# Kernel optimization log

Measured on AMD Instinct MI355X. Metric: run time of the kernel, lower is better.

The kernel has to match this reference:

```python
import jax, jax.numpy as jnp
import numpy as np
import math

D_MODEL = 1024
N_HEAD = 16
D_HEAD = D_MODEL // N_HEAD
SCALE = math.sqrt(D_HEAD)
B, S = 8, 512


def setup_inputs() -> dict:
    key = jax.random.key(0)
    ks = jax.random.split(key, 7)
    x = jax.random.normal(ks[0], (B, S, D_MODEL), dtype=jnp.float32)
    mask = jnp.ones((B, S), dtype=jnp.int32)
    qmask = jax.random.randint(ks[1], (B, S), 0, 2).astype(jnp.int32)
    # params
    Wqkv = jax.random.normal(ks[2], (4 * D_MODEL, D_MODEL), dtype=jnp.float32) / math.sqrt(D_MODEL)
    fc_w = jax.random.normal(ks[3], (D_MODEL, D_MODEL), dtype=jnp.float32) / math.sqrt(D_MODEL)
    fc_b = jnp.zeros((D_MODEL,), dtype=jnp.float32)
    shift = jnp.abs(jax.random.normal(ks[4], (1,), dtype=jnp.float32)) + 0.001
    bias = -jnp.abs(jax.random.normal(ks[5], (1,), dtype=jnp.float32))
    return {"x": x, "mask": mask, "qmask": qmask, "Wqkv": Wqkv,
            "fc_w": fc_w, "fc_b": fc_b, "shift": shift, "bias": bias}


def reference(x, mask, qmask, Wqkv, fc_w, fc_b, shift, bias):
    Bsz, L, D = x.shape
    qkv = x @ Wqkv.T  # [B,S,4D], no bias
    q, k1, k2, v = jnp.split(qkv, 4, axis=-1)

    def heads(t):  # [B,S,D] -> [B,H,S,dh]
        return t.reshape(Bsz, L, N_HEAD, D_HEAD).transpose(0, 2, 1, 3)

    q, k1, k2, v = heads(q), heads(k1), heads(k2), heads(v)

    attn_self = jnp.einsum('bhqd,bhkd->bhqk', q, k1)
    attn_others = jnp.einsum('bhqd,bhkd->bhqk', q, k2)
    same_spk = (qmask[:, :, None] == qmask[:, None, :])[:, None]  # [B,1,S,S]
    attn = jnp.where(same_spk, attn_self, attn_others) / SCALE

    # key padding mask
    attn = jnp.where((mask == 0)[:, None, None, :], -jnp.inf, attn)

    # Gaussian distance bias: -(shift*(i-j)^2 + bias)
    pos = jnp.arange(L, dtype=jnp.float32)
    sq_dist = (pos[:, None] - pos[None, :]) ** 2  # [S,S]
    attn = attn - (shift[0] * sq_dist + bias[0])

    p = jax.nn.softmax(attn, axis=-1)  # dropout=0 (eval)
    out = jnp.einsum('bhqk,bhkd->bhqd', p, v)
    out = out.transpose(0, 2, 1, 3).reshape(Bsz, L, D)
    return out @ fc_w.T + fc_b
```

## Files before the change

kernel.cpp:

```cpp
#include <hip/hip_runtime.h>

typedef unsigned short u16;
typedef __bf16 bf16_t;
typedef bf16_t bf16x8 __attribute__((ext_vector_type(8)));
typedef float f32x4 __attribute__((ext_vector_type(4)));
typedef u16 u16x8 __attribute__((ext_vector_type(8)));
typedef u16 u16x4 __attribute__((ext_vector_type(4)));

__device__ __forceinline__ u16 f2b(float f) {
    unsigned int u = __float_as_uint(f);
    u += 0x7fffu + ((u >> 16) & 1u);
    return (u16)(u >> 16);
}

__device__ __forceinline__ f32x4 mfma16(u16x8 a, u16x8 b, f32x4 c) {
    return __builtin_amdgcn_mfma_f32_16x16x32_bf16(
        __builtin_bit_cast(bf16x8, a), __builtin_bit_cast(bf16x8, b), c, 0, 0, 0);
}

#define GLDS16(gp, lp)                                                          \
    __builtin_amdgcn_global_load_lds(                                           \
        (const __attribute__((address_space(1))) void*)(gp),                    \
        (__attribute__((address_space(3))) void*)(lp), 16, 0, 0)

__global__ __launch_bounds__(256) void cvt3_kernel(const float* __restrict__ s0,
                                                   const float* __restrict__ s1,
                                                   const float* __restrict__ s2,
                                                   u16* __restrict__ d0,
                                                   u16* __restrict__ d1,
                                                   u16* __restrict__ d2) {
    int i = (blockIdx.x * 256 + threadIdx.x) * 4;
    const float* src; u16* dst;
    if (i < 4194304)       { src = s0;           dst = d0;           }
    else if (i < 8388608)  { src = s1 - 4194304; dst = d1 - 4194304; }
    else                   { src = s2 - 8388608; dst = d2 - 8388608; }
    float4 f = *(const float4*)(src + i);
    u16x4 o = { f2b(f.x), f2b(f.y), f2b(f.z), f2b(f.w) };
    *(u16x4*)(dst + i) = o;
}

template <int MT, int MODE>
__global__ __launch_bounds__(256) void gemm_bt(
    const u16* __restrict__ A, const u16* __restrict__ Bw,
    u16* __restrict__ Qf, u16* __restrict__ K1f,
    u16* __restrict__ K2f, u16* __restrict__ Vf,
    float* __restrict__ Cf, const float* __restrict__ biasp)
{
    constexpr int K = 1024;
    constexpr int MF = MT / 32;
    __shared__ u16 As[2][MT * 32];
    __shared__ u16 Bs[2][128 * 32];
    const int t = threadIdx.x;
    const int lane = t & 63;
    const int w = t >> 6;
    const int wm = w >> 1, wn = w & 1;
    const int lr = lane & 15, quad = lane >> 4;
    const int tileM = blockIdx.y * MT, tileN = blockIdx.x * 128;

    f32x4 acc[MF][4] = {};

    const u16* Ag = A + (size_t)(tileM + (t >> 2)) * K + (t & 3) * 8;
    const u16* Bg = Bw + (size_t)(tileN + (t >> 2)) * K + (t & 3) * 8;

#define STAGE(kk, bufi)                                                         \
    do {                                                                        \
        GLDS16(Ag + (kk), &As[bufi][t * 8]);                                    \
        if (MT == 128) GLDS16(Ag + (kk) + 64 * K, &As[bufi][t * 8 + 2048]);     \
        GLDS16(Bg + (kk), &Bs[bufi][t * 8]);                                    \
        GLDS16(Bg + (kk) + 64 * K, &Bs[bufi][t * 8 + 2048]);                    \
    } while (0)

    STAGE(0, 0);
    __syncthreads();

#pragma unroll 2
    for (int kk = 0; kk < K; kk += 32) {
        const int cur = (kk >> 5) & 1;
        if (kk + 32 < K) STAGE(kk + 32, cur ^ 1);

        u16x8 af[MF], bf[4];
#pragma unroll
        for (int i = 0; i < MF; ++i)
            af[i] = *(const u16x8*)(&As[cur][(wm * (MT / 2) + i * 16 + lr) * 32 + quad * 8]);
#pragma unroll
        for (int i = 0; i < 4; ++i)
            bf[i] = *(const u16x8*)(&Bs[cur][(wn * 64 + i * 16 + lr) * 32 + quad * 8]);
#pragma unroll
        for (int mi = 0; mi < MF; ++mi)
#pragma unroll
            for (int ni = 0; ni < 4; ++ni)
                acc[mi][ni] = mfma16(af[mi], bf[ni], acc[mi][ni]);

        __syncthreads();
    }
#undef STAGE

    if (MODE == 0) {
#pragma unroll
        for (int mi = 0; mi < MF; ++mi)
#pragma unroll
            for (int ni = 0; ni < 4; ++ni) {
                int n = tileN + wn * 64 + ni * 16 + lr;
                int kv = n >> 10;
                int h = (n >> 6) & 15, d = n & 63;
#pragma unroll
                for (int r = 0; r < 4; ++r) {
                    int m = tileM + wm * (MT / 2) + mi * 16 + quad * 4 + r;
                    int s = m & 511, bh = ((m >> 9) << 4) + h;
                    u16 v = f2b(acc[mi][ni][r]);
                    if (kv < 3) {
                        u16* base = (kv == 0) ? Qf : (kv == 1) ? K1f : K2f;
                        size_t idx = ((size_t)((bh * 32 + (s >> 4)) * 2 + (d >> 5))) * 512
                                   + (((d >> 3) & 3) * 16 + (s & 15)) * 8 + (d & 7);
                        base[idx] = v;
                    } else {
                        size_t idx = ((size_t)((bh * 4 + (d >> 4)) * 16 + (s >> 5))) * 512
                                   + (((s >> 3) & 3) * 16 + (d & 15)) * 8 + (s & 7);
                        Vf[idx] = v;
                    }
                }
            }
    } else {
#pragma unroll
        for (int mi = 0; mi < MF; ++mi)
#pragma unroll
            for (int ni = 0; ni < 4; ++ni) {
                int n = tileN + wn * 64 + ni * 16 + lr;
                float bv = biasp[n];
#pragma unroll
                for (int r = 0; r < 4; ++r) {
                    int m = tileM + wm * (MT / 2) + mi * 16 + quad * 4 + r;
                    Cf[(size_t)m * 1024 + n] = acc[mi][ni][r] + bv;
                }
            }
    }
}

__global__ __launch_bounds__(256) void attn_kernel(
    const u16* __restrict__ qfm, const u16* __restrict__ k1fm,
    const u16* __restrict__ k2fm, const u16* __restrict__ vfm,
    const int* __restrict__ maskp, const int* __restrict__ qmaskp,
    const float* __restrict__ shiftp, const float* __restrict__ biasp,
    u16* __restrict__ ao)
{
    __shared__ u16 Pw[4][2][512];

    const int bh = blockIdx.x & 127, qt = blockIdx.x >> 7;
    const int b = bh >> 4, h = bh & 15;
    const int t = threadIdx.x, lane = t & 63, w = t >> 6;
    const int lr = lane & 15, quad = lane >> 4;
    const float shiftv = shiftp[0], biasv = biasp[0];

    const int qbase = qt * 128 + w * 32;
    const int m16 = qbase >> 4;

    const u16* qb = qfm + ((size_t)(bh * 32 + m16) * 2) * 512 + lane * 8;
    u16x8 qa[2][2];
    qa[0][0] = *(const u16x8*)(qb);
    qa[0][1] = *(const u16x8*)(qb + 512);
    qa[1][0] = *(const u16x8*)(qb + 1024);
    qa[1][1] = *(const u16x8*)(qb + 1536);

    int qmr[2][4]; float rowf[2][4];
#pragma unroll
    for (int g = 0; g < 2; ++g)
#pragma unroll
        for (int r = 0; r < 4; ++r) {
            int m = qbase + g * 16 + quad * 4 + r;
            qmr[g][r] = qmaskp[b * 512 + m];
            rowf[g][r] = (float)m;
        }

    f32x4 o[2][4] = {};
    float lsum[2][4] = {};

    u16* pb[2] = { &Pw[w][0][0], &Pw[w][1][0] };
    const int wa0 = quad * 128 + (((lr >> 3) ^ quad) * 8) + (lr & 7);
    const int wa1 = quad * 128 + (((2 | (lr >> 3)) ^ quad) * 8) + (lr & 7);
    const int ra = lr * 32 + ((quad ^ (lr >> 2)) * 8);

    const u16* k1b = k1fm + (size_t)bh * 32768 + lane * 8;
    const u16* k2b = k2fm + (size_t)bh * 32768 + lane * 8;
    const u16* vb  = vfm  + (size_t)bh * 32768 + lane * 8;
    const int* qmb = qmaskp + b * 512;
    const int* kmb = maskp + b * 512;

#pragma unroll 2
    for (int cc = 0; cc < 16; ++cc) {
        const u16* kc1 = k1b + cc * 2048;
        const u16* kc2 = k2b + cc * 2048;
        u16x8 k1f_[2][2], k2f_[2][2];
        k1f_[0][0] = *(const u16x8*)(kc1);
        k1f_[0][1] = *(const u16x8*)(kc1 + 512);
        k1f_[1][0] = *(const u16x8*)(kc1 + 1024);
        k1f_[1][1] = *(const u16x8*)(kc1 + 1536);
        k2f_[0][0] = *(const u16x8*)(kc2);
        k2f_[0][1] = *(const u16x8*)(kc2 + 512);
        k2f_[1][0] = *(const u16x8*)(kc2 + 1024);
        k2f_[1][1] = *(const u16x8*)(kc2 + 1536);
        u16x8 vf_[4];
#pragma unroll
        for (int ot = 0; ot < 4; ++ot)
            vf_[ot] = *(const u16x8*)(vb + (size_t)(ot * 16 + cc) * 512);

        f32x4 z = {0.f, 0.f, 0.f, 0.f};
        f32x4 s1[2][2], s2[2][2];
#pragma unroll
        for (int g = 0; g < 2; ++g)
#pragma unroll
            for (int tg = 0; tg < 2; ++tg) {
                s1[g][tg] = mfma16(qa[g][1], k1f_[tg][1], mfma16(qa[g][0], k1f_[tg][0], z));
                s2[g][tg] = mfma16(qa[g][1], k2f_[tg][1], mfma16(qa[g][0], k2f_[tg][0], z));
            }

        const int col0 = cc * 32 + lr, col1 = col0 + 16;
        const int qmc0 = qmb[col0], qmc1 = qmb[col1];
        const float ka0 = (kmb[col0] ? 0.f : -1e30f) - 10.0f;
        const float ka1 = (kmb[col1] ? 0.f : -1e30f) - 10.0f;
        const float colf0 = (float)col0, colf1 = (float)col1;

#pragma unroll
        for (int g = 0; g < 2; ++g) {
#pragma unroll
            for (int r = 0; r < 4; ++r) {
                float d0 = rowf[g][r] - colf0;
                float d1 = rowf[g][r] - colf1;
                float sel0 = (qmr[g][r] == qmc0) ? s1[g][0][r] : s2[g][0][r];
                float sel1 = (qmr[g][r] == qmc1) ? s1[g][1][r] : s2[g][1][r];
                float v0 = fmaf(sel0, 0.125f, -fmaf(shiftv * d0, d0, biasv)) + ka0;
                float v1 = fmaf(sel1, 0.125f, -fmaf(shiftv * d1, d1, biasv)) + ka1;
                float p0 = __expf(v0);
                float p1 = __expf(v1);
                lsum[g][r] += p0 + p1;
                pb[g][wa0 + r * 32] = f2b(p0);
                pb[g][wa1 + r * 32] = f2b(p1);
            }
        }
#pragma unroll
        for (int g = 0; g < 2; ++g) {
            u16x8 af = *(const u16x8*)(pb[g] + ra);
#pragma unroll
            for (int ot = 0; ot < 4; ++ot)
                o[g][ot] = mfma16(af, vf_[ot], o[g][ot]);
        }
    }

#pragma unroll
    for (int g = 0; g < 2; ++g)
#pragma unroll
        for (int r = 0; r < 4; ++r) {
            float s = lsum[g][r];
#pragma unroll
            for (int m = 1; m < 16; m <<= 1) s += __shfl_xor(s, m);
            float inv = 1.0f / s;
            int grow = b * 512 + qbase + g * 16 + quad * 4 + r;
            u16* orow = ao + (size_t)grow * 1024 + h * 64 + lr;
            orow[0]  = f2b(o[g][0][r] * inv);
            orow[16] = f2b(o[g][1][r] * inv);
            orow[32] = f2b(o[g][2][r] * inv);
            orow[48] = f2b(o[g][3][r] * inv);
        }
}

extern "C" void kernel_launch(void* const* d_in, const int* in_sizes, int n_in,
                              void* d_out, int out_size, void* d_ws, size_t ws_size,
                              hipStream_t stream) {
    (void)in_sizes; (void)n_in; (void)out_size; (void)ws_size;
    const float* x      = (const float*)d_in[0];
    const int*   maskp  = (const int*)d_in[1];
    const int*   qmaskp = (const int*)d_in[2];
    const float* Wqkv   = (const float*)d_in[3];
    const float* fc_w   = (const float*)d_in[4];
    const float* fc_b   = (const float*)d_in[5];
    const float* shiftp = (const float*)d_in[6];
    const float* biasp  = (const float*)d_in[7];
    float* out = (float*)d_out;

    char* ws = (char*)d_ws;
    u16* xb   = (u16*)(ws);
    u16* wb   = (u16*)(ws + (8u << 20));
    u16* fwb  = (u16*)(ws + (16u << 20));
    u16* qfm  = (u16*)(ws + (18u << 20));
    u16* k1fm = (u16*)(ws + (26u << 20));
    u16* k2fm = (u16*)(ws + (34u << 20));
    u16* vfm  = (u16*)(ws + (42u << 20));
    u16* aob  = (u16*)(ws + (50u << 20));

    cvt3_kernel<<<9216, 256, 0, stream>>>(x, Wqkv, fc_w, xb, wb, fwb);
    gemm_bt<128, 0><<<dim3(32, 32), 256, 0, stream>>>(xb, wb, qfm, k1fm, k2fm, vfm,
                                                      nullptr, nullptr);
    attn_kernel<<<512, 256, 0, stream>>>(qfm, k1fm, k2fm, vfm, maskp, qmaskp,
                                         shiftp, biasp, aob);
    gemm_bt<64, 1><<<dim3(8, 64), 256, 0, stream>>>(aob, fwb, nullptr, nullptr,
                                                    nullptr, nullptr, out, fc_b);
}
```

Measured before the change: 205.0 us.

## Swap GEMM operand roles for QKV tiles to write packed bf16 fragments

In the QKV projection GEMM, blocks producing Q/K1/K2 swap which shared-memory tile feeds the A and B MFMA operands, so each lane's accumulator holds consecutive head-dim elements. Lanes can then pack four bf16 values into one 8-byte store instead of scattered 2-byte stores. The V blocks likewise use vectorized packed stores, and the attention kernel's fragment-layout addressing changes to match the new intermediate layout. This targets the costly scattered epilogue writes in the projection, at the cost of layout coupling that depends on specific grid dimensions.

```diff
diff --git a/kernel.cpp b/kernel.cpp
--- a/kernel.cpp
+++ b/kernel.cpp
@@ -11,6 +11,9 @@
     unsigned int u = __float_as_uint(f);
     u += 0x7fffu + ((u >> 16) & 1u);
     return (u16)(u >> 16);
+}
+__device__ __forceinline__ unsigned int pk2(float a, float b) {
+    return (unsigned int)f2b(a) | ((unsigned int)f2b(b) << 16);
 }
 
 __device__ __forceinline__ f32x4 mfma16(u16x8 a, u16x8 b, f32x4 c) {
@@ -62,6 +65,12 @@
     const u16* Ag = A + (size_t)(tileM + (t >> 2)) * K + (t & 3) * 8;
     const u16* Bg = Bw + (size_t)(tileN + (t >> 2)) * K + (t & 3) * 8;
 
+    const bool swp = (MODE == 0) && (blockIdx.x < 24);
+    const u16* Afb = swp ? &Bs[0][0] : &As[0][0];
+    const u16* Bfb = swp ? &As[0][0] : &Bs[0][0];
+    const int AfS = swp ? 128 * 32 : MT * 32;
+    const int BfS = swp ? MT * 32 : 128 * 32;
+
 #define STAGE(kk, bufi)                                                         \
     do {                                                                        \
         GLDS16(Ag + (kk), &As[bufi][t * 8]);                                    \
@@ -81,10 +90,10 @@
         u16x8 af[MF], bf[4];
 #pragma unroll
         for (int i = 0; i < MF; ++i)
-            af[i] = *(const u16x8*)(&As[cur][(wm * (MT / 2) + i * 16 + lr) * 32 + quad * 8]);
+            af[i] = *(const u16x8*)(Afb + cur * AfS + (wm * (MT / 2) + i * 16 + lr) * 32 + quad * 8);
 #pragma unroll
         for (int i = 0; i < 4; ++i)
-            bf[i] = *(const u16x8*)(&Bs[cur][(wn * 64 + i * 16 + lr) * 32 + quad * 8]);
+            bf[i] = *(const u16x8*)(Bfb + cur * BfS + (wn * 64 + i * 16 + lr) * 32 + quad * 8);
 #pragma unroll
         for (int mi = 0; mi < MF; ++mi)
 #pragma unroll
@@ -96,30 +105,37 @@
 #undef STAGE
 
     if (MODE == 0) {
-#pragma unroll
-        for (int mi = 0; mi < MF; ++mi)
-#pragma unroll
-            for (int ni = 0; ni < 4; ++ni) {
-                int n = tileN + wn * 64 + ni * 16 + lr;
-                int kv = n >> 10;
-                int h = (n >> 6) & 15, d = n & 63;
-#pragma unroll
-                for (int r = 0; r < 4; ++r) {
-                    int m = tileM + wm * (MT / 2) + mi * 16 + quad * 4 + r;
-                    int s = m & 511, bh = ((m >> 9) << 4) + h;
-                    u16 v = f2b(acc[mi][ni][r]);
-                    if (kv < 3) {
-                        u16* base = (kv == 0) ? Qf : (kv == 1) ? K1f : K2f;
-                        size_t idx = ((size_t)((bh * 32 + (s >> 4)) * 2 + (d >> 5))) * 512
-                                   + (((d >> 3) & 3) * 16 + (s & 15)) * 8 + (d & 7);
-                        base[idx] = v;
-                    } else {
-                        size_t idx = ((size_t)((bh * 4 + (d >> 4)) * 16 + (s >> 5))) * 512
-                                   + (((s >> 3) & 3) * 16 + (d & 15)) * 8 + (s & 7);
-                        Vf[idx] = v;
-                    }
+        if (swp) {
+            const int kvi = blockIdx.x >> 3;
+            const int h = ((blockIdx.x & 7) << 1) + wm;
+            const int bh = ((blockIdx.y >> 2) << 4) + h;
+            const int t16b = ((blockIdx.y & 3) << 3) + wn * 4;
+            u16* bp = (kvi == 0 ? Qf : (kvi == 1 ? K1f : K2f))
+                    + ((size_t)(bh * 32 + t16b) * 2) * 512 + lr * 32 + quad * 4;
+#pragma unroll
+            for (int mi = 0; mi < MF; ++mi)
+#pragma unroll
+                for (int ni = 0; ni < 4; ++ni) {
+                    uint2 v;
+                    v.x = pk2(acc[mi][ni][0], acc[mi][ni][1]);
+                    v.y = pk2(acc[mi][ni][2], acc[mi][ni][3]);
+                    *(uint2*)(bp + ni * 1024 + (mi >> 1) * 512 + (mi & 1) * 16) = v;
                 }
-            }
+        } else {
+            const int h = ((blockIdx.x - 24) << 1) + wn;
+            const int bh = ((blockIdx.y >> 2) << 4) + h;
+            const int t5b = ((blockIdx.y & 3) << 2) + wm * 2;
+            u16* bp = Vf + ((size_t)(bh * 4) * 16 + t5b) * 512 + lr * 32 + quad * 4;
+#pragma unroll
+            for (int mi = 0; mi < MF; ++mi)
+#pragma unroll
+                for (int ni = 0; ni < 4; ++ni) {
+                    uint2 v;
+                    v.x = pk2(acc[mi][ni][0], acc[mi][ni][1]);
+                    v.y = pk2(acc[mi][ni][2], acc[mi][ni][3]);
+                    *(uint2*)(bp + ni * 8192 + (mi >> 1) * 512 + (mi & 1) * 16) = v;
+                }
+        }
     } else {
 #pragma unroll
         for (int mi = 0; mi < MF; ++mi)
@@ -153,8 +169,9 @@
 
     const int qbase = qt * 128 + w * 32;
     const int m16 = qbase >> 4;
-
-    const u16* qb = qfm + ((size_t)(bh * 32 + m16) * 2) * 512 + lane * 8;
+    const int loff = lr * 32 + quad * 8;
+
+    const u16* qb = qfm + ((size_t)(bh * 32 + m16) * 2) * 512 + loff;
     u16x8 qa[2][2];
     qa[0][0] = *(const u16x8*)(qb);
     qa[0][1] = *(const u16x8*)(qb + 512);
@@ -179,9 +196,9 @@
     const int wa1 = quad * 128 + (((2 | (lr >> 3)) ^ quad) * 8) + (lr & 7);
     const int ra = lr * 32 + ((quad ^ (lr >> 2)) * 8);
 
-    const u16* k1b = k1fm + (size_t)bh * 32768 + lane * 8;
-    const u16* k2b = k2fm + (size_t)bh * 32768 + lane * 8;
-    const u16* vb  = vfm  + (size_t)bh * 32768 + lane * 8;
+    const u16* k1b = k1fm + (size_t)bh * 32768 + loff;
+    const u16* k2b = k2fm + (size_t)bh * 32768 + loff;
+    const u16* vb  = vfm  + (size_t)bh * 32768 + loff;
     const int* qmb = qmaskp + b * 512;
     const int* kmb = maskp + b * 512;
 
```

After: 204.7 us. About the same (-0.2%).
